# Optimization experiments

Hardware: AMD Instinct MI355X
Metric: run time of the kernel (lower is better)

The kernel has to match this reference:

```python
import jax, jax.numpy as jnp
import numpy as np

N = 100000        # nodes
DEG = 16          # fixed neighbor count per node
E = N * DEG       # total edges
D = 128           # node feature dim
DE = 16           # edge feature dim
DOUT = 128


def setup_inputs() -> dict:
    key = jax.random.key(0)
    k1, k2, k3, k4, k5 = jax.random.split(key, 5)
    h = jax.random.normal(k1, (N, D), dtype=jnp.float32)
    edge_table = jax.random.normal(k2, (E, DE), dtype=jnp.float32)
    # xavier-uniform-ish init for W (2D + DE, DOUT)
    fan_in, fan_out = 2 * D + DE, DOUT
    limit = float(np.sqrt(6.0 / (fan_in + fan_out)))
    W = jax.random.uniform(k3, (fan_in, fan_out), dtype=jnp.float32,
                           minval=-limit, maxval=limit)
    neighbor_idx = jax.random.randint(k4, (E,), 0, N, dtype=jnp.int64)
    edge_idx = jax.random.randint(k5, (E,), 0, E, dtype=jnp.int64)
    segment_ids = jnp.repeat(jnp.arange(N, dtype=jnp.int64), DEG)  # sorted, fixed degree
    return {"h": h, "edge_table": edge_table, "W": W,
            "neighbor_idx": neighbor_idx, "edge_idx": edge_idx,
            "segment_ids": segment_ids}


def reference(h, edge_table, W, neighbor_idx, edge_idx, segment_ids):
    # ragged gather: per-edge neighbor node feats + edge feats -> [E, D+DE]
    nf = jnp.take(h, neighbor_idx, axis=0)                 # [E, D]
    ef = jnp.take(edge_table, edge_idx, axis=0)            # [E, DE]
    cat = jnp.concatenate([nf, ef], axis=1)                # [E, D+DE]
    # per-node segment mean (ragged reduce)
    sums = jax.ops.segment_sum(cat, segment_ids, num_segments=N)          # [N, D+DE]
    counts = jax.ops.segment_sum(jnp.ones((cat.shape[0], 1), cat.dtype),
                                 segment_ids, num_segments=N)             # [N, 1]
    mean = sums / jnp.maximum(counts, 1.0)
    feat = jnp.concatenate([h, mean], axis=1)              # [N, 2D+DE]
    return jax.nn.elu(feat @ W)                            # [N, DOUT]
```

## Files before the change

### kernel.cpp

```cpp
#include <hip/hip_runtime.h>
#include <cstdint>

#define NNODES 100000
#define NDEG 16
#define DFEAT 128
#define DEDGE 16
#define KDIM  272
#define KPAD  288
#define NDOUT 128
#define NKSTEP 9

typedef __attribute__((ext_vector_type(8))) short bf16x8;
typedef __attribute__((ext_vector_type(4))) short s16x4;
typedef __attribute__((ext_vector_type(4))) float f32x4;

__device__ __forceinline__ unsigned short f32_to_bf16_rn(float x) {
    union { float f; unsigned u; } v; v.f = x;
    unsigned r = v.u + 0x7FFF + ((v.u >> 16) & 1);
    return (unsigned short)(r >> 16);
}
__device__ __forceinline__ float bf16_bits_to_f32(unsigned short b) {
    union { unsigned u; float f; } v; v.u = ((unsigned)b) << 16; return v.f;
}

__global__ __launch_bounds__(256) void prep_h_kernel(
    const float* __restrict__ h, short* __restrict__ A)
{
    int t = blockIdx.x * 256 + threadIdx.x;
    if (t >= NNODES * 16) return;
    int n  = t >> 4;
    int c8 = t & 15;
    const float4* __restrict__ h4 = (const float4*)h;
    float4 v0 = h4[(size_t)n * 32 + c8 * 2];
    float4 v1 = h4[(size_t)n * 32 + c8 * 2 + 1];
    bf16x8 o;
    o[0] = (short)f32_to_bf16_rn(v0.x); o[1] = (short)f32_to_bf16_rn(v0.y);
    o[2] = (short)f32_to_bf16_rn(v0.z); o[3] = (short)f32_to_bf16_rn(v0.w);
    o[4] = (short)f32_to_bf16_rn(v1.x); o[5] = (short)f32_to_bf16_rn(v1.y);
    o[6] = (short)f32_to_bf16_rn(v1.z); o[7] = (short)f32_to_bf16_rn(v1.w);
    *(bf16x8*)(A + (size_t)n * KPAD + c8 * 8) = o;
}

__global__ __launch_bounds__(256) void wt_pack_kernel(
    const float* __restrict__ W, short* __restrict__ Bh, short* __restrict__ Bl)
{
    int t = blockIdx.x * 256 + threadIdx.x;
    if (t >= NKSTEP * 8 * 64) return;
    int c   = t >> 9;
    int rem = t & 511;
    int n   = rem >> 6;
    int l   = rem & 63;
    int col = n * 16 + (l & 15);
    int kb  = l >> 4;
    bf16x8 hv, lv;
#pragma unroll
    for (int j = 0; j < 8; ++j) {
        int k = c * 32 + kb * 8 + j;
        float val = (k < KDIM) ? W[(size_t)k * NDOUT + col] : 0.0f;
        unsigned short hi = f32_to_bf16_rn(val);
        unsigned short lo = f32_to_bf16_rn(val - bf16_bits_to_f32(hi));
        hv[j] = (short)hi; lv[j] = (short)lo;
    }
    *(bf16x8*)(Bh + (size_t)t * 8) = hv;
    *(bf16x8*)(Bl + (size_t)t * 8) = lv;
}

__global__ __launch_bounds__(256) void agg_kernel(
    short* __restrict__ A, const float* __restrict__ et,
    const int* __restrict__ nidx, const int* __restrict__ eidx)
{
    int gwave = (blockIdx.x * 256 + threadIdx.x) >> 6;
    int lane  = threadIdx.x & 63;
    if (gwave >= NNODES) return;
    const int n = gwave;
    const int c8 = lane & 15;
    const int g  = lane >> 4;
    const float inv = 1.0f / 16.0f;

    float acc[8];
#pragma unroll
    for (int j = 0; j < 8; ++j) acc[j] = 0.f;
#pragma unroll
    for (int t = 0; t < 4; ++t) {
        int nbr = nidx[n * NDEG + t * 4 + g];
        bf16x8 v = *(const bf16x8*)(A + (size_t)nbr * KPAD + c8 * 8);
#pragma unroll
        for (int j = 0; j < 8; ++j) acc[j] += bf16_bits_to_f32((unsigned short)v[j]);
    }
#pragma unroll
    for (int j = 0; j < 8; ++j) {
        acc[j] += __shfl_xor(acc[j], 16);
        acc[j] += __shfl_xor(acc[j], 32);
    }
    if (g == 0) {
        bf16x8 o;
#pragma unroll
        for (int j = 0; j < 8; ++j) o[j] = (short)f32_to_bf16_rn(acc[j] * inv);
        *(bf16x8*)(A + (size_t)n * KPAD + DFEAT + c8 * 8) = o;
    }

    const float4* __restrict__ et4 = (const float4*)et;
    int ke = lane >> 2, q = lane & 3;
    int e = eidx[n * NDEG + ke];
    float4 ev = et4[(size_t)e * (DEDGE / 4) + q];
#pragma unroll
    for (int m = 4; m < 64; m <<= 1) {
        ev.x += __shfl_xor(ev.x, m);
        ev.y += __shfl_xor(ev.y, m);
        ev.z += __shfl_xor(ev.z, m);
        ev.w += __shfl_xor(ev.w, m);
    }
    if (lane < 4) {
        s16x4 o;
        o[0] = (short)f32_to_bf16_rn(ev.x * inv);
        o[1] = (short)f32_to_bf16_rn(ev.y * inv);
        o[2] = (short)f32_to_bf16_rn(ev.z * inv);
        o[3] = (short)f32_to_bf16_rn(ev.w * inv);
        *(s16x4*)(A + (size_t)n * KPAD + 256 + lane * 4) = o;
    }
    if (lane == 4) *(bf16x8*)(A + (size_t)n * KPAD + 272) = (bf16x8)0;
    if (lane == 5) *(bf16x8*)(A + (size_t)n * KPAD + 280) = (bf16x8)0;
}

__global__ __launch_bounds__(256) void gemm_kernel(
    const short* __restrict__ A, const short* __restrict__ Bh,
    const short* __restrict__ Bl, float* __restrict__ out)
{
    const int tid  = threadIdx.x;
    const int wave = tid >> 6;
    const int lane = tid & 63;
    const int m0   = blockIdx.x * 128 + wave * 32;
    const int m    = lane & 15;
    const int kb   = lane >> 4;

    int r0 = m0 + m;      if (r0 >= NNODES) r0 = NNODES - 1;
    int r1 = m0 + 16 + m; if (r1 >= NNODES) r1 = NNODES - 1;

    const short* pa0 = A + (size_t)r0 * KPAD + kb * 8;
    const short* pa1 = A + (size_t)r1 * KPAD + kb * 8;

    f32x4 acc0[8], acc1[8];
#pragma unroll
    for (int n = 0; n < 8; ++n) {
        acc0[n] = (f32x4){0.f, 0.f, 0.f, 0.f};
        acc1[n] = (f32x4){0.f, 0.f, 0.f, 0.f};
    }

#pragma unroll
    for (int c = 0; c < NKSTEP; ++c) {
        bf16x8 a0 = *(const bf16x8*)(pa0 + c * 32);
        bf16x8 a1 = *(const bf16x8*)(pa1 + c * 32);
        const short* pb = (const short*)((size_t)(c * 8) * 64 * 8 + (size_t)lane * 8);
#pragma unroll
        for (int n = 0; n < 8; ++n) {
            size_t off = ((size_t)(c * 8 + n) * 64 + lane) * 8;
            bf16x8 bh = *(const bf16x8*)(Bh + off);
            bf16x8 bl = *(const bf16x8*)(Bl + off);
            acc0[n] = __builtin_amdgcn_mfma_f32_16x16x32_bf16(a0, bh, acc0[n], 0, 0, 0);
            acc0[n] = __builtin_amdgcn_mfma_f32_16x16x32_bf16(a0, bl, acc0[n], 0, 0, 0);
            acc1[n] = __builtin_amdgcn_mfma_f32_16x16x32_bf16(a1, bh, acc1[n], 0, 0, 0);
            acc1[n] = __builtin_amdgcn_mfma_f32_16x16x32_bf16(a1, bl, acc1[n], 0, 0, 0);
        }
        (void)pb;
    }

    const int colb   = lane & 15;
    const int rbase0 = m0 + ((lane >> 4) << 2);
#pragma unroll
    for (int n = 0; n < 8; ++n) {
#pragma unroll
        for (int r = 0; r < 4; ++r) {
            int row = rbase0 + r;
            if (row < NNODES) {
                float v = acc0[n][r];
                v = v > 0.f ? v : expm1f(v);
                out[(size_t)row * NDOUT + n * 16 + colb] = v;
            }
            int row1 = rbase0 + 16 + r;
            if (row1 < NNODES) {
                float v = acc1[n][r];
                v = v > 0.f ? v : expm1f(v);
                out[(size_t)row1 * NDOUT + n * 16 + colb] = v;
            }
        }
    }
}

extern "C" void kernel_launch(void* const* d_in, const int* in_sizes, int n_in,
                              void* d_out, int out_size, void* d_ws, size_t ws_size,
                              hipStream_t stream)
{
    const float* h    = (const float*)d_in[0];
    const float* et   = (const float*)d_in[1];
    const float* W    = (const float*)d_in[2];
    const int*   nidx = (const int*)d_in[3];
    const int*   eidx = (const int*)d_in[4];

    short* A  = (short*)d_ws;
    short* Bh = A + (size_t)NNODES * KPAD;
    short* Bl = Bh + (size_t)NKSTEP * 8 * 64 * 8;
    float* out = (float*)d_out;

    wt_pack_kernel<<<(NKSTEP * 8 * 64 + 255) / 256, 256, 0, stream>>>(W, Bh, Bl);
    prep_h_kernel<<<(NNODES * 16 + 255) / 256, 256, 0, stream>>>(h, A);
    agg_kernel<<<(NNODES * 64 + 255) / 256, 256, 0, stream>>>(A, et, nidx, eidx);
    gemm_kernel<<<(NNODES + 127) / 128, 256, 0, stream>>>(A, Bh, Bl, out);
}
```

Before: 345.1 us.

## Keep W fragments in registers and stage A tile through LDS in GEMM

The GEMM is restructured so that each wave owns 32 output columns and keeps its slice of the split-bf16 weight fragments (hi and lo) resident in registers across the K dimension. The block's 64-row A tile is loaded once into shared memory and shared by all four waves. Previously every wave re-read all of B from global/L2 for each 32-row chunk. This removes most of the redundant B traffic at the cost of higher register pressure (36 bf16x8 B fragments per lane), a block-wide sync, and twice as many blocks.

```diff
diff --git a/kernel.cpp b/kernel.cpp
--- a/kernel.cpp
+++ b/kernel.cpp
@@ -122,68 +122,73 @@
     if (lane == 5) *(bf16x8*)(A + (size_t)n * KPAD + 280) = (bf16x8)0;
 }
 
-__global__ __launch_bounds__(256) void gemm_kernel(
+__global__ __launch_bounds__(256, 2) void gemm_kernel(
     const short* __restrict__ A, const short* __restrict__ Bh,
     const short* __restrict__ Bl, float* __restrict__ out)
 {
+    __shared__ short sA[4 * NKSTEP * 64 * 8];
+
     const int tid  = threadIdx.x;
-    const int wave = tid >> 6;
+    const int w    = tid >> 6;
     const int lane = tid & 63;
-    const int m0   = blockIdx.x * 128 + wave * 32;
-    const int m    = lane & 15;
-    const int kb   = lane >> 4;
-
-    int r0 = m0 + m;      if (r0 >= NNODES) r0 = NNODES - 1;
-    int r1 = m0 + 16 + m; if (r1 >= NNODES) r1 = NNODES - 1;
-
-    const short* pa0 = A + (size_t)r0 * KPAD + kb * 8;
-    const short* pa1 = A + (size_t)r1 * KPAD + kb * 8;
-
-    f32x4 acc0[8], acc1[8];
-#pragma unroll
-    for (int n = 0; n < 8; ++n) {
-        acc0[n] = (f32x4){0.f, 0.f, 0.f, 0.f};
-        acc1[n] = (f32x4){0.f, 0.f, 0.f, 0.f};
-    }
-
-#pragma unroll
-    for (int c = 0; c < NKSTEP; ++c) {
-        bf16x8 a0 = *(const bf16x8*)(pa0 + c * 32);
-        bf16x8 a1 = *(const bf16x8*)(pa1 + c * 32);
-        const short* pb = (const short*)((size_t)(c * 8) * 64 * 8 + (size_t)lane * 8);
-#pragma unroll
-        for (int n = 0; n < 8; ++n) {
-            size_t off = ((size_t)(c * 8 + n) * 64 + lane) * 8;
-            bf16x8 bh = *(const bf16x8*)(Bh + off);
-            bf16x8 bl = *(const bf16x8*)(Bl + off);
-            acc0[n] = __builtin_amdgcn_mfma_f32_16x16x32_bf16(a0, bh, acc0[n], 0, 0, 0);
-            acc0[n] = __builtin_amdgcn_mfma_f32_16x16x32_bf16(a0, bl, acc0[n], 0, 0, 0);
-            acc1[n] = __builtin_amdgcn_mfma_f32_16x16x32_bf16(a1, bh, acc1[n], 0, 0, 0);
-            acc1[n] = __builtin_amdgcn_mfma_f32_16x16x32_bf16(a1, bl, acc1[n], 0, 0, 0);
+    const int m0   = blockIdx.x * 64;
+
+    bf16x8 bh[2][NKSTEP], bl[2][NKSTEP];
+#pragma unroll
+    for (int n = 0; n < 2; ++n)
+#pragma unroll
+        for (int c = 0; c < NKSTEP; ++c) {
+            size_t off = ((size_t)(c * 8 + (w * 2 + n)) * 64 + lane) * 8;
+            bh[n][c] = *(const bf16x8*)(Bh + off);
+            bl[n][c] = *(const bf16x8*)(Bl + off);
         }
-        (void)pb;
-    }
-
-    const int colb   = lane & 15;
-    const int rbase0 = m0 + ((lane >> 4) << 2);
-#pragma unroll
-    for (int n = 0; n < 8; ++n) {
-#pragma unroll
-        for (int r = 0; r < 4; ++r) {
-            int row = rbase0 + r;
-            if (row < NNODES) {
-                float v = acc0[n][r];
-                v = v > 0.f ? v : expm1f(v);
-                out[(size_t)row * NDOUT + n * 16 + colb] = v;
-            }
-            int row1 = rbase0 + 16 + r;
-            if (row1 < NNODES) {
-                float v = acc1[n][r];
-                v = v > 0.f ? v : expm1f(v);
-                out[(size_t)row1 * NDOUT + n * 16 + colb] = v;
+
+    {
+        const int g = (tid >> 4) & 3;
+        const int i = tid & 15;
+        int row = m0 + w * 16 + i;
+        if (row >= NNODES) row = NNODES - 1;
+        const short* src = A + (size_t)row * KPAD + g * 8;
+        short* dst = sA + ((size_t)(w * NKSTEP) * 64 + lane) * 8;
+#pragma unroll
+        for (int p = 0; p < NKSTEP; ++p)
+            *(bf16x8*)(dst + (size_t)p * 64 * 8) = *(const bf16x8*)(src + p * 32);
+    }
+    __syncthreads();
+
+    f32x4 acc[2][4];
+#pragma unroll
+    for (int n = 0; n < 2; ++n)
+#pragma unroll
+        for (int f = 0; f < 4; ++f) acc[n][f] = (f32x4){0.f, 0.f, 0.f, 0.f};
+
+#pragma unroll
+    for (int f = 0; f < 4; ++f)
+#pragma unroll
+        for (int c = 0; c < NKSTEP; ++c) {
+            bf16x8 a = *(const bf16x8*)(sA + ((size_t)(f * NKSTEP + c) * 64 + lane) * 8);
+#pragma unroll
+            for (int n = 0; n < 2; ++n) {
+                acc[n][f] = __builtin_amdgcn_mfma_f32_16x16x32_bf16(a, bh[n][c], acc[n][f], 0, 0, 0);
+                acc[n][f] = __builtin_amdgcn_mfma_f32_16x16x32_bf16(a, bl[n][c], acc[n][f], 0, 0, 0);
             }
         }
-    }
+
+    const int colb = w * 32 + (lane & 15);
+    const int rsub = (lane >> 4) << 2;
+#pragma unroll
+    for (int n = 0; n < 2; ++n)
+#pragma unroll
+        for (int f = 0; f < 4; ++f)
+#pragma unroll
+            for (int r = 0; r < 4; ++r) {
+                int row = m0 + f * 16 + rsub + r;
+                if (row < NNODES) {
+                    float v = acc[n][f][r];
+                    v = v > 0.f ? v : expm1f(v);
+                    out[(size_t)row * NDOUT + colb + n * 16] = v;
+                }
+            }
 }
 
 extern "C" void kernel_launch(void* const* d_in, const int* in_sizes, int n_in,
@@ -204,5 +209,5 @@
     wt_pack_kernel<<<(NKSTEP * 8 * 64 + 255) / 256, 256, 0, stream>>>(W, Bh, Bl);
     prep_h_kernel<<<(NNODES * 16 + 255) / 256, 256, 0, stream>>>(h, A);
     agg_kernel<<<(NNODES * 64 + 255) / 256, 256, 0, stream>>>(A, et, nidx, eidx);
-    gemm_kernel<<<(NNODES + 127) / 128, 256, 0, stream>>>(A, Bh, Bl, out);
-}
+    gemm_kernel<<<(NNODES + 63) / 64, 256, 0, stream>>>(A, Bh, Bl, out);
+}
```

New measurement: 314.0 us. 1.1x faster.
